# Kernel tuning notes

Measured on AMD Instinct MI355X. Metric: run time of the kernel, lower is better.

Reference implementation:

```python
import jax, jax.numpy as jnp
import numpy as np

H = 16  # num_heads


def setup_inputs() -> dict:
    key = jax.random.key(0)
    ks = jax.random.split(key, 8)
    B, S, d, L = 1, 2048, 1024, 8
    hd = d // H
    s = 0.02
    return {
        "x": jax.random.normal(ks[0], (B, S, d), jnp.float32),
        "past_values": jax.random.normal(ks[1], (L, B, H, S, hd), jnp.float32),
        "Wqkv": jax.random.normal(ks[2], (3 * d, d), jnp.float32) * s,
        "bqkv": jax.random.normal(ks[3], (3 * d,), jnp.float32) * s,
        "Wcol": jax.random.normal(ks[4], (d, d), jnp.float32) * s,
        "bcol": jax.random.normal(ks[5], (d,), jnp.float32) * s,
        "Wout": jax.random.normal(ks[6], (d, d), jnp.float32) * s,
        "bout": jax.random.normal(ks[7], (d,), jnp.float32) * s,
    }


def reference(x, past_values, Wqkv, bqkv, Wcol, bcol, Wout, bout):
    B, S, d = x.shape
    L = past_values.shape[0]
    hd = d // H
    scale = 1.0 / np.sqrt(hd).astype(np.float32)

    qkv = x @ Wqkv.T + bqkv                       # [B,S,3d]
    q, k, v = jnp.split(qkv, 3, axis=-1)

    def heads(t):                                  # [B,S,d] -> [B,H,S,hd]
        return t.reshape(B, S, H, hd).transpose(0, 2, 1, 3)

    q_row, k, v = heads(q), heads(k), heads(v)
    q_col = heads(x @ Wcol.T + bcol)

    # causal token scores [B,H,S,S]
    token_scores = jnp.einsum('bhqd,bhkd->bhqk', q_row, k) * scale
    causal = jnp.triu(jnp.ones((S, S), bool), 1)
    token_scores = jnp.where(causal, -jnp.inf, token_scores)

    # stack past values: torch stack(dim=3) -> [B,H,S,L,hd]; permute -> [B,S,L,H*hd]
    pv = past_values.transpose(1, 3, 0, 2, 4).reshape(B, S, L, d)
    ri = pv.reshape(B, S * L, d)
    mu = ri.mean(-1, keepdims=True)
    var = ri.var(-1, keepdims=True)
    ri = (ri - mu) / jnp.sqrt(var + 1e-5)          # F.layer_norm, no affine

    Wk, bk = Wqkv[d:2 * d], bqkv[d:2 * d]
    Wv, bv = Wqkv[2 * d:], bqkv[2 * d:]
    rk = (ri @ Wk.T + bk).reshape(B, S * L, H, hd).transpose(0, 2, 1, 3).reshape(B, H, S, L, hd)
    rv = (ri @ Wv.T + bv).reshape(B, S * L, H, hd).transpose(0, 2, 1, 3).reshape(B, H, S, L, hd)

    mem_scores = jnp.einsum('bhsd,bhsld->bhsl', q_col, rk) * scale  # [B,H,S,L]

    scores = jnp.concatenate([token_scores, mem_scores], axis=-1)   # [B,H,S,S+L]
    w = jax.nn.softmax(scores, axis=-1)
    tw, mw = w[..., :S], w[..., S:]

    ctx = jnp.einsum('bhqk,bhkd->bhqd', tw, v) + jnp.einsum('bhsl,bhsld->bhsd', mw, rv)
    out = ctx.transpose(0, 2, 1, 3).reshape(B, S, d)
    return out @ Wout.T + bout
```

## Files before the change

### kernel.cpp

```cpp
#include <hip/hip_runtime.h>
#include <math.h>

#define D   1024
#define H   16
#define HD  64
#define SEQ 2048
#define LL  8
#define SCALE 0.125f

typedef __attribute__((ext_vector_type(8))) __bf16 bf16x8;
typedef __attribute__((ext_vector_type(4))) float floatx4;
typedef __attribute__((ext_vector_type(8))) unsigned short ushort8;

__device__ inline unsigned short f32_to_bf16(float f) {
    unsigned int u = __builtin_bit_cast(unsigned int, f);
    u += 0x7FFF + ((u >> 16) & 1);
    return (unsigned short)(u >> 16);
}
__device__ inline float bf2f(unsigned short u) {
    unsigned int x = (unsigned int)u << 16;
    return __builtin_bit_cast(float, x);
}
__device__ inline void load_lds16(const void* g, void* l) {
    __builtin_amdgcn_global_load_lds(
        (__attribute__((address_space(1))) void*)g,
        (__attribute__((address_space(3))) void*)l, 16, 0, 0);
}

__device__ inline void xcd_swizzle(int& bx, int& by) {
    const int gx   = gridDim.x;
    const int lin  = blockIdx.y * gx + blockIdx.x;
    const int nblk = gx * gridDim.y;
    const int virt = (lin & 7) * (nblk >> 3) + (lin >> 3);
    bx = virt % gx;
    by = virt / gx;
}

#define NQ_X    524288
#define NQ_WQKV 786432
#define NQ_WC   262144
#define NQ_WO   262144
#define LN_BLK  16384
#define CVT_BLK 7168
#define PREP_GRID (LN_BLK + CVT_BLK + 4)

__global__ __launch_bounds__(256) void prep_kernel(
    const float* __restrict__ pv, const float* __restrict__ x,
    const float* __restrict__ Wqkv, const float* __restrict__ Wcol,
    const float* __restrict__ Wout, const float* __restrict__ bqkv,
    const float* __restrict__ bcol,
    unsigned short* __restrict__ ri, unsigned short* __restrict__ xb,
    unsigned short* __restrict__ W4b, unsigned short* __restrict__ Woutb,
    float* __restrict__ b4)
{
    const int b = blockIdx.x;
    const int t = threadIdx.x;
    if (b < LN_BLK) {
        const int r = b;
        const int s = r >> 3, l = r & 7;
        const int h = t >> 4, e = (t & 15) * 4;
        const size_t src = (size_t)l * (H * SEQ * HD) + (size_t)h * (SEQ * HD)
                         + (size_t)s * HD + e;
        float4 v = *(const float4*)(pv + src);
        float sum = v.x + v.y + v.z + v.w;
        float sq  = v.x * v.x + v.y * v.y + v.z * v.z + v.w * v.w;
#pragma unroll
        for (int off = 32; off; off >>= 1) {
            sum += __shfl_xor(sum, off);
            sq  += __shfl_xor(sq, off);
        }
        __shared__ float red[8];
        if ((t & 63) == 0) { red[(t >> 6) * 2] = sum; red[(t >> 6) * 2 + 1] = sq; }
        __syncthreads();
        sum = red[0] + red[2] + red[4] + red[6];
        sq  = red[1] + red[3] + red[5] + red[7];
        const float mean = sum * (1.f / 1024.f);
        const float var  = sq * (1.f / 1024.f) - mean * mean;
        const float rstd = rsqrtf(var + 1e-5f);
        ushort4 o;
        o.x = f32_to_bf16((v.x - mean) * rstd);
        o.y = f32_to_bf16((v.y - mean) * rstd);
        o.z = f32_to_bf16((v.z - mean) * rstd);
        o.w = f32_to_bf16((v.w - mean) * rstd);
        *(ushort4*)(ri + (size_t)r * D + t * 4) = o;
    } else if (b < LN_BLK + CVT_BLK) {
        const int i = (b - LN_BLK) * 256 + t;
        const float* src; unsigned short* dst; int off;
        if (i < NQ_X)                        { src = x;    dst = xb;    off = i; }
        else if (i < NQ_X + NQ_WQKV)         { src = Wqkv; dst = W4b;   off = i - NQ_X; }
        else if (i < NQ_X + NQ_WQKV + NQ_WC) {
            float4 v = ((const float4*)Wcol)[i - NQ_X - NQ_WQKV];
            ushort4 o;
            o.x = f32_to_bf16(v.x); o.y = f32_to_bf16(v.y);
            o.z = f32_to_bf16(v.z); o.w = f32_to_bf16(v.w);
            ((ushort4*)(W4b))[NQ_WQKV + (i - NQ_X - NQ_WQKV)] = o;
            return;
        }
        else                                 { src = Wout; dst = Woutb; off = i - NQ_X - NQ_WQKV - NQ_WC; }
        float4 v = ((const float4*)src)[off];
        ushort4 o;
        o.x = f32_to_bf16(v.x); o.y = f32_to_bf16(v.y);
        o.z = f32_to_bf16(v.z); o.w = f32_to_bf16(v.w);
        ((ushort4*)dst)[off] = o;
    } else {
        const int q = (b - LN_BLK - CVT_BLK) * 256 + t;
        float4 v = (q < 768) ? ((const float4*)bqkv)[q] : ((const float4*)bcol)[q - 768];
        ((float4*)b4)[q] = v;
    }
}

__global__ __launch_bounds__(256) void wkt_kernel(
    const float* __restrict__ Wqkv, unsigned short* __restrict__ WkT)
{
    const int h = blockIdx.x >> 4, ct = blockIdx.x & 15;
    const int c0 = ct * 64;
    const int t = threadIdx.x;
    __shared__ float tile[64][68];
    {
        const int e  = t >> 2;
        const int c4 = (t & 3) * 16;
        const float* src = Wqkv + (size_t)(D + h * HD + e) * D + c0 + c4;
#pragma unroll
        for (int j = 0; j < 4; j++) {
            float4 v = ((const float4*)src)[j];
            *(float4*)&tile[e][c4 + j * 4] = v;
        }
    }
    __syncthreads();
    {
        const int c  = t >> 2;
        const int e0 = (t & 3) * 16;
        ushort8 o0, o1;
#pragma unroll
        for (int j = 0; j < 8; j++) o0[j] = f32_to_bf16(tile[e0 + j][c]);
#pragma unroll
        for (int j = 0; j < 8; j++) o1[j] = f32_to_bf16(tile[e0 + 8 + j][c]);
        unsigned short* dst = WkT + (size_t)h * (D * HD) + (size_t)(c0 + c) * HD + e0;
        *(ushort8*)dst       = o0;
        *(ushort8*)(dst + 8) = o1;
    }
}

template <typename CT, bool HAS_BIAS>
__global__ __launch_bounds__(256) void gemm_bf16_kernel(
    const unsigned short* __restrict__ A, const unsigned short* __restrict__ W,
    const float* __restrict__ bias, CT* __restrict__ C,
    int K, int N, int lda, int ldw, int ldc,
    size_t zsA, size_t zsW, size_t zsC)
{
    A += (size_t)blockIdx.z * zsA;
    W += (size_t)blockIdx.z * zsW;
    C += (size_t)blockIdx.z * zsC;

    __shared__ unsigned short As[128 * 32];
    __shared__ unsigned short Ws[128 * 32];
    const int t    = threadIdx.x;
    const int wave = t >> 6, lane = t & 63;
    const int wm   = wave >> 1, wn = wave & 1;
    int bx, by;
    xcd_swizzle(bx, by);
    const int m0 = by * 128, n0 = bx * 128;

    floatx4 acc[4][4];
#pragma unroll
    for (int i = 0; i < 4; i++)
#pragma unroll
        for (int j = 0; j < 4; j++) acc[i][j] = (floatx4)0.f;

    const int lrow = lane >> 2;
    const int lcol = (lane & 3) * 8;
    const unsigned short* Ag = A + (size_t)(m0 + wave * 32 + lrow) * lda + lcol;
    const unsigned short* Wg = W + (size_t)(n0 + wave * 32 + lrow) * ldw + lcol;
    unsigned short* Asw = &As[wave * 32 * 32];
    unsigned short* Wsw = &Ws[wave * 32 * 32];
    const size_t rowskipA = (size_t)16 * lda;
    const size_t rowskipW = (size_t)16 * ldw;

    const int arow  = lane & 15;
    const int aquad = (lane >> 4) * 8;

    for (int k0 = 0; k0 < K; k0 += 32) {
        load_lds16(Ag + k0,             Asw);
        load_lds16(Ag + k0 + rowskipA,  Asw + 16 * 32);
        load_lds16(Wg + k0,             Wsw);
        load_lds16(Wg + k0 + rowskipW,  Wsw + 16 * 32);
        __syncthreads();

        bf16x8 af[4], wf[4];
#pragma unroll
        for (int mi = 0; mi < 4; mi++)
            af[mi] = *(const bf16x8*)&As[(wm * 64 + mi * 16 + arow) * 32 + aquad];
#pragma unroll
        for (int ni = 0; ni < 4; ni++)
            wf[ni] = *(const bf16x8*)&Ws[(wn * 64 + ni * 16 + arow) * 32 + aquad];
#pragma unroll
        for (int mi = 0; mi < 4; mi++)
#pragma unroll
            for (int ni = 0; ni < 4; ni++)
                acc[mi][ni] = __builtin_amdgcn_mfma_f32_16x16x32_bf16(
                    af[mi], wf[ni], acc[mi][ni], 0, 0, 0);
        __syncthreads();
    }

    const int crow = (lane >> 4) * 4, ccol = lane & 15;
#pragma unroll
    for (int mi = 0; mi < 4; mi++) {
#pragma unroll
        for (int ni = 0; ni < 4; ni++) {
            const int gm = m0 + wm * 64 + mi * 16 + crow;
            const int gn = n0 + wn * 64 + ni * 16 + ccol;
            float bb = 0.f;
            if constexpr (HAS_BIAS) bb = bias[gn];
#pragma unroll
            for (int r = 0; r < 4; r++) {
                float v = acc[mi][ni][r] + bb;
                if constexpr (sizeof(CT) == 2)
                    C[(size_t)(gm + r) * ldc + gn] = (CT)f32_to_bf16(v);
                else
                    C[(size_t)(gm + r) * ldc + gn] = v;
            }
        }
    }
}

#define RI_STRIDE 1032

__global__ __launch_bounds__(256) void memsc_kernel(
    const unsigned short* __restrict__ U, const unsigned short* __restrict__ ri,
    const unsigned short* __restrict__ qkv4, const float* __restrict__ bqkv,
    float* __restrict__ scores)
{
    const int s = blockIdx.x;
    const int t = threadIdx.x;
    __shared__ unsigned short riS[LL * RI_STRIDE];
    __shared__ float qbS[H];
    {
        const unsigned short* src = ri + (size_t)s * (LL * D);
#pragma unroll
        for (int j = 0; j < 4; j++) {
            const int off = (j * 256 + t) * 8;
            const int l = off >> 10, c = off & 1023;
            ushort8 v = *(const ushort8*)(src + off);
            *(ushort8*)&riS[l * RI_STRIDE + c] = v;
        }
    }
    {
        const int h = t >> 4, sub = t & 15;
        const unsigned short* qc = qkv4 + (size_t)s * 4096 + 3 * D + h * HD + sub * 4;
        const float* bk = bqkv + D + h * HD + sub * 4;
        float acc = 0.f;
#pragma unroll
        for (int j = 0; j < 4; j++) acc += bf2f(qc[j]) * bk[j];
#pragma unroll
        for (int off = 1; off < 16; off <<= 1) acc += __shfl_xor(acc, off);
        if (sub == 0) qbS[h] = acc;
    }
    __syncthreads();
    const int p = t >> 1, half = t & 1;
    const int h = p >> 3, l = p & 7;
    const unsigned short* Up = U + ((size_t)h * SEQ + s) * D + half * 512;
    const unsigned short* rp = &riS[l * RI_STRIDE + half * 512];
    float acc = 0.f;
#pragma unroll 4
    for (int j = 0; j < 64; j++) {
        ushort8 u = *(const ushort8*)(Up + j * 8);
        ushort8 r = *(const ushort8*)(rp + j * 8);
#pragma unroll
        for (int k = 0; k < 8; k++) acc += bf2f(u[k]) * bf2f(r[k]);
    }
    acc += __shfl_xor(acc, 1);
    if (half == 0)
        scores[((size_t)s * H + h) * LL + l] = (acc + qbS[h]) * SCALE;
}

union AttnShared {
    struct { unsigned short Qs[64 * 72]; unsigned short Ks[64 * 72]; } qk;
    float Osp[64 * 68];
};

__global__ __launch_bounds__(256) void attn_split_kernel(
    const unsigned short* __restrict__ qkv4,
    const float* __restrict__ mem_scores, float* __restrict__ memP,
    float* __restrict__ Opart, float2* __restrict__ mlpart)
{
    const int t    = threadIdx.x;
    const int w    = t >> 6, lane = t & 63;
    const int lrow = lane & 15;
    const int lk   = (lane >> 4) * 8;
    const int rrow = (lane >> 4) * 4;
    const int lin  = blockIdx.x;
    const int hs   = lin & 31, g = lin >> 5;
    const int h    = hs >> 1, s = hs & 1;
    const int a    = g & 7, bq = g >> 3;
    const int qt   = (bq == 0) ? a : (bq == 1) ? 15 - a : (bq == 2) ? 16 + a : 31 - a;
    const int q0   = qt * 64;
    const int n    = qt + 1, nh = (n + 1) >> 1;
    const int lo   = s ? nh : 0, hi = s ? n : nh;
    const int part = (h * 32 + qt) * 2 + s;

    __shared__ AttnShared U;
    __shared__ unsigned short Vt[64 * 72];
    __shared__ unsigned short Pb[64 * 72];
    __shared__ float row_m[64], row_l[64];
    __shared__ float mem_mm[64], mem_alpha[64], mem_suml[64];

#pragma unroll
    for (int p = 0; p < 2; p++) {
        int idx = p * 256 + t;
        int row = idx >> 3, col = (idx & 7) * 8;
        *(bf16x8*)&U.qk.Qs[row * 72 + col] =
            *(const bf16x8*)(qkv4 + (size_t)(q0 + row) * 4096 + h * HD + col);
    }

    float m_i[4], l_i[4];
    floatx4 Oacc[4];
#pragma unroll
    for (int r = 0; r < 4; r++) { m_i[r] = -1e30f; l_i[r] = 0.f; }
#pragma unroll
    for (int et = 0; et < 4; et++) Oacc[et] = (floatx4)0.f;

    for (int jt = lo; jt < hi; jt++) {
        const int j0 = jt * 64;
#pragma unroll
        for (int p = 0; p < 2; p++) {
            int idx = p * 256 + t;
            int row = idx >> 3, col = (idx & 7) * 8;
            *(bf16x8*)&U.qk.Ks[row * 72 + col] =
                *(const bf16x8*)(qkv4 + (size_t)(j0 + row) * 4096 + D + h * HD + col);
        }
        {
            const int pr = t & 31, eg = t >> 5;
            const unsigned short* v0 =
                qkv4 + (size_t)(j0 + 2 * pr) * 4096 + 2 * D + h * HD + eg * 8;
            ushort8 va = *(const ushort8*)v0;
            ushort8 vb = *(const ushort8*)(v0 + 4096);
#pragma unroll
            for (int j = 0; j < 8; j++) {
                unsigned int pk = (unsigned int)va[j] | ((unsigned int)vb[j] << 16);
                *(unsigned int*)&Vt[(eg * 8 + j) * 72 + 2 * pr] = pk;
            }
        }
        __syncthreads();

        floatx4 S[4];
#pragma unroll
        for (int nt = 0; nt < 4; nt++) S[nt] = (floatx4)0.f;
#pragma unroll
        for (int kst = 0; kst < 2; kst++) {
            bf16x8 aq = *(const bf16x8*)&U.qk.Qs[(w * 16 + lrow) * 72 + kst * 32 + lk];
#pragma unroll
            for (int nt = 0; nt < 4; nt++) {
                bf16x8 bk = *(const bf16x8*)&U.qk.Ks[(nt * 16 + lrow) * 72 + kst * 32 + lk];
                S[nt] = __builtin_amdgcn_mfma_f32_16x16x32_bf16(aq, bk, S[nt], 0, 0, 0);
            }
        }

#pragma unroll
        for (int r = 0; r < 4; r++) {
            const int qg = q0 + w * 16 + rrow + r;
            float sc[4];
            float mx = -1e30f;
#pragma unroll
            for (int nt = 0; nt < 4; nt++) {
                sc[nt] = S[nt][r] * SCALE;
                if (j0 + nt * 16 + lrow > qg) sc[nt] = -1e30f;
                mx = fmaxf(mx, sc[nt]);
            }
#pragma unroll
            for (int off = 1; off < 16; off <<= 1)
                mx = fmaxf(mx, __shfl_xor(mx, off));
            if (mx <= -1e29f) {
#pragma unroll
                for (int nt = 0; nt < 4; nt++)
                    Pb[(w * 16 + rrow + r) * 72 + nt * 16 + lrow] = 0;
                continue;
            }
            const float newm  = fmaxf(m_i[r], mx);
            const float alpha = __expf(m_i[r] - newm);
            m_i[r] = newm;
            float ps = 0.f;
#pragma unroll
            for (int nt = 0; nt < 4; nt++) {
                float pe = __expf(sc[nt] - newm);
                ps += pe;
                Pb[(w * 16 + rrow + r) * 72 + nt * 16 + lrow] = f32_to_bf16(pe);
            }
#pragma unroll
            for (int off = 1; off < 16; off <<= 1)
                ps += __shfl_xor(ps, off);
            l_i[r] = l_i[r] * alpha + ps;
#pragma unroll
            for (int et = 0; et < 4; et++) Oacc[et][r] *= alpha;
        }
        __syncthreads();

#pragma unroll
        for (int kst = 0; kst < 2; kst++) {
            bf16x8 ap = *(const bf16x8*)&Pb[(w * 16 + lrow) * 72 + kst * 32 + lk];
#pragma unroll
            for (int et = 0; et < 4; et++) {
                bf16x8 bv = *(const bf16x8*)&Vt[(et * 16 + lrow) * 72 + kst * 32 + lk];
                Oacc[et] = __builtin_amdgcn_mfma_f32_16x16x32_bf16(ap, bv, Oacc[et], 0, 0, 0);
            }
        }
        __syncthreads();
    }

    if (s == 1) {
#pragma unroll
        for (int r = 0; r < 4; r++) {
            const int ql = w * 16 + rrow + r;
            if (lrow == 0) mlpart[(size_t)part * 64 + ql] = make_float2(m_i[r], l_i[r]);
#pragma unroll
            for (int et = 0; et < 4; et++)
                Opart[((size_t)part * 64 + ql) * 64 + et * 16 + lrow] = Oacc[et][r];
        }
        return;
    }

#pragma unroll
    for (int r = 0; r < 4; r++) {
        const int ql = w * 16 + rrow + r;
        if (lrow == 0) { row_m[ql] = m_i[r]; row_l[ql] = l_i[r]; }
#pragma unroll
        for (int et = 0; et < 4; et++)
            U.Osp[ql * 68 + et * 16 + lrow] = Oacc[et][r];
    }
    __syncthreads();

    if (t < 64) {
        const int qi = t, qg = q0 + qi;
        const float* msp = mem_scores + ((size_t)qg * H + h) * LL;
        float ms[LL];
#pragma unroll
        for (int l = 0; l < LL; l++) ms[l] = msp[l];
        const float mo = row_m[qi];
        float mm = mo;
#pragma unroll
        for (int l = 0; l < LL; l++) mm = fmaxf(mm, ms[l]);
        const float alpha = __expf(mo - mm);
        float suml = 0.f;
        float* mp = memP + ((size_t)qg * H + h) * LL;
#pragma unroll
        for (int l = 0; l < LL; l++) {
            float pe = __expf(ms[l] - mm);
            suml += pe;
            mp[l] = pe;
        }
        mem_mm[qi] = mm; mem_alpha[qi] = alpha; mem_suml[qi] = suml;
    }
    __syncthreads();

    {
        const int tx = t & 15, ty = t >> 4;
#pragma unroll
        for (int i = 0; i < 4; i++) {
            const int qi = ty * 4 + i;
            const float alpha = mem_alpha[qi];
            const float lf = row_l[qi] * alpha + mem_suml[qi];
            float4 o = *(const float4*)&U.Osp[qi * 68 + tx * 4];
            o.x *= alpha; o.y *= alpha; o.z *= alpha; o.w *= alpha;
            *(float4*)&Opart[((size_t)part * 64 + qi) * 64 + tx * 4] = o;
            if (tx == 0) mlpart[(size_t)part * 64 + qi] = make_float2(mem_mm[qi], lf);
        }
    }
}

__global__ __launch_bounds__(256) void attn_merge_kernel(
    const float* __restrict__ Opart, const float2* __restrict__ mlpart,
    const float* __restrict__ memP,
    float* __restrict__ tok, float* __restrict__ mwf, float* __restrict__ Pmem)
{
    const int blk = blockIdx.x;
    const int h = blk >> 5, qt = blk & 31;
    const int q0 = qt * 64;
    const int t = threadIdx.x, tx = t & 15, ty = t >> 4;
    const size_t p0 = (size_t)blk * 2, p1 = p0 + 1;
#pragma unroll
    for (int i = 0; i < 4; i++) {
        const int qi = ty * 4 + i, qg = q0 + qi;
        float2 ml0 = mlpart[p0 * 64 + qi];
        float2 ml1 = mlpart[p1 * 64 + qi];
        const float M  = fmaxf(ml0.x, ml1.x);
        const float f0 = __expf(ml0.x - M), f1 = __expf(ml1.x - M);
        const float rl = 1.f / (ml0.y * f0 + ml1.y * f1);
        float4 o0 = *(const float4*)&Opart[(p0 * 64 + qi) * 64 + tx * 4];
        float4 o1 = *(const float4*)&Opart[(p1 * 64 + qi) * 64 + tx * 4];
        float4 o;
        o.x = (o0.x * f0 + o1.x * f1) * rl;
        o.y = (o0.y * f0 + o1.y * f1) * rl;
        o.z = (o0.z * f0 + o1.z * f1) * rl;
        o.w = (o0.w * f0 + o1.w * f1) * rl;
        *(float4*)&tok[(size_t)qg * D + h * HD + tx * 4] = o;
        if (tx == 0) {
            const float w0 = f0 * rl;
            const float* mp = memP + ((size_t)qg * H + h) * LL;
            float* mw = mwf + ((size_t)qg * H + h) * LL;
            float psum = 0.f;
#pragma unroll
            for (int l = 0; l < LL; l++) { float v = mp[l] * w0; mw[l] = v; psum += v; }
            Pmem[(size_t)qg * H + h] = psum;
        }
    }
}

__global__ __launch_bounds__(256) void rbar_kernel(
    const float* __restrict__ mwf, const unsigned short* __restrict__ ri,
    unsigned short* __restrict__ rbar)
{
    const int s = blockIdx.x, t = threadIdx.x;
    __shared__ unsigned short riS[LL * D];
    __shared__ float wS[H * LL];
    {
        const unsigned short* src = ri + (size_t)s * (LL * D);
#pragma unroll
        for (int j = 0; j < 4; j++) {
            const int off = (j * 256 + t) * 8;
            *(ushort8*)&riS[off] = *(const ushort8*)(src + off);
        }
    }
    if (t < H * LL) wS[t] = mwf[(size_t)s * (H * LL) + t];
    __syncthreads();
    const int c4 = t * 4;
#pragma unroll
    for (int hh = 0; hh < H; hh++) {
        float v0 = 0.f, v1 = 0.f, v2 = 0.f, v3 = 0.f;
#pragma unroll
        for (int l = 0; l < LL; l++) {
            const float wv = wS[hh * LL + l];
            ushort4 rr = *(const ushort4*)&riS[l * D + c4];
            v0 += wv * bf2f(rr.x); v1 += wv * bf2f(rr.y);
            v2 += wv * bf2f(rr.z); v3 += wv * bf2f(rr.w);
        }
        ushort4 o;
        o.x = f32_to_bf16(v0); o.y = f32_to_bf16(v1);
        o.z = f32_to_bf16(v2); o.w = f32_to_bf16(v3);
        *(ushort4*)(rbar + ((size_t)hh * SEQ + s) * D + c4) = o;
    }
}

__global__ __launch_bounds__(256) void gemm_ctx_kernel(
    const unsigned short* __restrict__ rbar, const unsigned short* __restrict__ W4,
    const float* __restrict__ bqkv, const float* __restrict__ Pmem,
    const float* __restrict__ tok, unsigned short* __restrict__ ctx)
{
    const int mt = blockIdx.x;
    const int h  = blockIdx.y;
    const unsigned short* A  = rbar + (size_t)h * SEQ * D + (size_t)mt * 128 * D;
    const unsigned short* Wv = W4 + (size_t)(2 * D + h * HD) * D;
    const float* bv = bqkv + 2 * D + h * HD;

    __shared__ unsigned short As[128 * 32];
    __shared__ unsigned short Ws[64 * 32];
    const int t    = threadIdx.x;
    const int wave = t >> 6, lane = t & 63;

    floatx4 acc[2][4];
#pragma unroll
    for (int i = 0; i < 2; i++)
#pragma unroll
        for (int j = 0; j < 4; j++) acc[i][j] = (floatx4)0.f;

    const int lrow = lane >> 2;
    const int lcol = (lane & 3) * 8;
    const unsigned short* Ag = A  + (size_t)(wave * 32 + lrow) * D + lcol;
    const unsigned short* Wg = Wv + (size_t)(wave * 32 + lrow) * D + lcol;
    unsigned short* Asw = &As[wave * 32 * 32];
    unsigned short* Wsw = &Ws[wave * 32 * 32];
    const size_t rowskip = (size_t)16 * D;

    const int arow  = lane & 15;
    const int aquad = (lane >> 4) * 8;

    for (int k0 = 0; k0 < D; k0 += 32) {
        load_lds16(Ag + k0,           Asw);
        load_lds16(Ag + k0 + rowskip, Asw + 16 * 32);
        if (wave < 2) {
            load_lds16(Wg + k0,           Wsw);
            load_lds16(Wg + k0 + rowskip, Wsw + 16 * 32);
        }
        __syncthreads();

        bf16x8 af[2], wf[4];
#pragma unroll
        for (int mi = 0; mi < 2; mi++)
            af[mi] = *(const bf16x8*)&As[(wave * 32 + mi * 16 + arow) * 32 + aquad];
#pragma unroll
        for (int ni = 0; ni < 4; ni++)
            wf[ni] = *(const bf16x8*)&Ws[(ni * 16 + arow) * 32 + aquad];
#pragma unroll
        for (int mi = 0; mi < 2; mi++)
#pragma unroll
            for (int ni = 0; ni < 4; ni++)
                acc[mi][ni] = __builtin_amdgcn_mfma_f32_16x16x32_bf16(
                    af[mi], wf[ni], acc[mi][ni], 0, 0, 0);
        __syncthreads();
    }

    const int crow = (lane >> 4) * 4, ccol = lane & 15;
#pragma unroll
    for (int mi = 0; mi < 2; mi++) {
#pragma unroll
        for (int ni = 0; ni < 4; ni++) {
            const int e  = ni * 16 + ccol;
            const float bb = bv[e];
#pragma unroll
            for (int r = 0; r < 4; r++) {
                const int grow = mt * 128 + wave * 32 + mi * 16 + crow + r;
                float v = acc[mi][ni][r] + bb * Pmem[(size_t)grow * H + h]
                          + tok[(size_t)grow * D + h * HD + e];
                ctx[(size_t)grow * D + h * HD + e] = f32_to_bf16(v);
            }
        }
    }
}

extern "C" void kernel_launch(void* const* d_in, const int* in_sizes, int n_in,
                              void* d_out, int out_size, void* d_ws, size_t ws_size,
                              hipStream_t stream)
{
    const float* x    = (const float*)d_in[0];
    const float* pv   = (const float*)d_in[1];
    const float* Wqkv = (const float*)d_in[2];
    const float* bqkv = (const float*)d_in[3];
    const float* Wcol = (const float*)d_in[4];
    const float* bcol = (const float*)d_in[5];
    const float* Wout = (const float*)d_in[6];
    const float* bout = (const float*)d_in[7];
    float* out = (float*)d_out;

    char* p = (char*)d_ws;
    unsigned short* x_bf    = (unsigned short*)p; p += (size_t)2048 * 1024 * 2;
    unsigned short* W4_bf   = (unsigned short*)p; p += (size_t)4096 * 1024 * 2;
    unsigned short* Wout_bf = (unsigned short*)p; p += (size_t)1024 * 1024 * 2;
    float*          b4      = (float*)p;          p += (size_t)4096 * 4;
    unsigned short* ri_bf   = (unsigned short*)p; p += (size_t)16384 * 1024 * 2;
    unsigned short* qkv4_bf = (unsigned short*)p; p += (size_t)2048 * 4096 * 2;
    unsigned short* WkT_bf  = (unsigned short*)p; p += (size_t)16 * 1024 * 64 * 2;
    float*          scores  = (float*)p;          p += (size_t)2048 * 16 * 8 * 4;
    float*          memP    = (float*)p;          p += (size_t)2048 * 16 * 8 * 4;
    float*          mwf     = (float*)p;          p += (size_t)2048 * 16 * 8 * 4;
    float*          Pmem    = (float*)p;          p += (size_t)2048 * 16 * 4;
    float*          tok     = (float*)p;          p += (size_t)2048 * 1024 * 4;
    unsigned short* ctx_bf  = (unsigned short*)p; p += (size_t)2048 * 1024 * 2;
    float*          Opart   = (float*)p;          p += (size_t)1024 * 64 * 64 * 4;
    float2*         mlpart  = (float2*)p;         p += (size_t)1024 * 64 * 8;
    unsigned short* Urb     = (unsigned short*)p; p += (size_t)16 * 2048 * 1024 * 2;

    prep_kernel<<<PREP_GRID, 256, 0, stream>>>(pv, x, Wqkv, Wcol, Wout, bqkv, bcol,
                                               ri_bf, x_bf, W4_bf, Wout_bf, b4);
    wkt_kernel<<<256, 256, 0, stream>>>(Wqkv, WkT_bf);
    gemm_bf16_kernel<unsigned short, true><<<dim3(32, 16, 1), 256, 0, stream>>>(
        x_bf, W4_bf, b4, qkv4_bf, 1024, 4096, 1024, 1024, 4096, 0, 0, 0);
    gemm_bf16_kernel<unsigned short, false><<<dim3(8, 16, 16), 256, 0, stream>>>(
        qkv4_bf + 3 * D, WkT_bf, nullptr, Urb, 64, 1024, 4096, 64, 1024,
        (size_t)HD, (size_t)D * HD, (size_t)SEQ * D);
    memsc_kernel<<<2048, 256, 0, stream>>>(Urb, ri_bf, qkv4_bf, bqkv, scores);
    attn_split_kernel<<<1024, 256, 0, stream>>>(qkv4_bf, scores, memP, Opart, mlpart);
    attn_merge_kernel<<<512, 256, 0, stream>>>(Opart, mlpart, memP, tok, mwf, Pmem);
    rbar_kernel<<<2048, 256, 0, stream>>>(mwf, ri_bf, Urb);
    gemm_ctx_kernel<<<dim3(16, 16), 256, 0, stream>>>(Urb, W4_bf, bqkv, Pmem, tok, ctx_bf);
    gemm_bf16_kernel<float, true><<<dim3(8, 16, 1), 256, 0, stream>>>(
        ctx_bf, Wout_bf, bout, out, 1024, 1024, 1024, 1024, 1024, 0, 0, 0);
}
```

Before: 365.5 us.

## Split attention KV range four ways with register-prefetched K/V and Q in registers

The causal attention kernel now splits each (head, query-tile) KV range into four parts instead of two, doubling the grid to 2048 blocks, and the merge kernel combines four partials. Q fragments are held in registers rather than LDS. The next K/V tile is prefetched into registers while the current tile is computed. MFMA sections are wrapped in s_setprio, and the final partial output is written straight from registers instead of staged through shared memory. The aim is better load balance and latency hiding in the attention stage, at the cost of more partial-result traffic, more register pressure, and a heavier merge.

Measured after the change: 343.7 us. -5.9%, faster.

```diff
diff --git a/kernel.cpp b/kernel.cpp
--- a/kernel.cpp
+++ b/kernel.cpp
@@ -273,11 +273,6 @@
         scores[((size_t)s * H + h) * LL + l] = (acc + qbS[h]) * SCALE;
 }
 
-union AttnShared {
-    struct { unsigned short Qs[64 * 72]; unsigned short Ks[64 * 72]; } qk;
-    float Osp[64 * 68];
-};
-
 __global__ __launch_bounds__(256) void attn_split_kernel(
     const unsigned short* __restrict__ qkv4,
     const float* __restrict__ mem_scores, float* __restrict__ memP,
@@ -289,28 +284,30 @@
     const int lk   = (lane >> 4) * 8;
     const int rrow = (lane >> 4) * 4;
     const int lin  = blockIdx.x;
-    const int hs   = lin & 31, g = lin >> 5;
-    const int h    = hs >> 1, s = hs & 1;
+    const int hsp  = lin & 63, g = lin >> 6;
+    const int h    = hsp >> 2, s = hsp & 3;
     const int a    = g & 7, bq = g >> 3;
     const int qt   = (bq == 0) ? a : (bq == 1) ? 15 - a : (bq == 2) ? 16 + a : 31 - a;
     const int q0   = qt * 64;
-    const int n    = qt + 1, nh = (n + 1) >> 1;
-    const int lo   = s ? nh : 0, hi = s ? n : nh;
-    const int part = (h * 32 + qt) * 2 + s;
-
-    __shared__ AttnShared U;
+    const int n    = qt + 1;
+    const int lo   = (s * n) >> 2, hi = ((s + 1) * n) >> 2;
+    const int part = (h * 32 + qt) * 4 + s;
+
+    __shared__ unsigned short Ks[64 * 72];
     __shared__ unsigned short Vt[64 * 72];
     __shared__ unsigned short Pb[64 * 72];
     __shared__ float row_m[64], row_l[64];
     __shared__ float mem_mm[64], mem_alpha[64], mem_suml[64];
 
-#pragma unroll
-    for (int p = 0; p < 2; p++) {
-        int idx = p * 256 + t;
-        int row = idx >> 3, col = (idx & 7) * 8;
-        *(bf16x8*)&U.qk.Qs[row * 72 + col] =
-            *(const bf16x8*)(qkv4 + (size_t)(q0 + row) * 4096 + h * HD + col);
-    }
+    bf16x8 qreg[2];
+#pragma unroll
+    for (int kst = 0; kst < 2; kst++)
+        qreg[kst] = *(const bf16x8*)(qkv4 + (size_t)(q0 + w * 16 + lrow) * 4096
+                                     + h * HD + kst * 32 + lk);
+
+    bf16x8 kr[2];
+    ushort8 va, vb;
+    const int vpr = t & 31, veg = t >> 5;
 
     float m_i[4], l_i[4];
     floatx4 Oacc[4];
@@ -319,41 +316,58 @@
 #pragma unroll
     for (int et = 0; et < 4; et++) Oacc[et] = (floatx4)0.f;
 
+    const int krow = (t >> 3);
+    const int kcol = (t & 7) * 8;
+
+    if (lo < hi) {
+        const int j0 = lo * 64;
+#pragma unroll
+        for (int p = 0; p < 2; p++)
+            kr[p] = *(const bf16x8*)(qkv4 + (size_t)(j0 + p * 32 + krow) * 4096
+                                     + D + h * HD + kcol);
+        const unsigned short* v0 =
+            qkv4 + (size_t)(j0 + 2 * vpr) * 4096 + 2 * D + h * HD + veg * 8;
+        va = *(const ushort8*)v0;
+        vb = *(const ushort8*)(v0 + 4096);
+#pragma unroll
+        for (int p = 0; p < 2; p++)
+            *(bf16x8*)&Ks[(p * 32 + krow) * 72 + kcol] = kr[p];
+#pragma unroll
+        for (int j = 0; j < 8; j++) {
+            unsigned int pk = (unsigned int)va[j] | ((unsigned int)vb[j] << 16);
+            *(unsigned int*)&Vt[(veg * 8 + j) * 72 + 2 * vpr] = pk;
+        }
+        __syncthreads();
+    }
+
     for (int jt = lo; jt < hi; jt++) {
         const int j0 = jt * 64;
-#pragma unroll
-        for (int p = 0; p < 2; p++) {
-            int idx = p * 256 + t;
-            int row = idx >> 3, col = (idx & 7) * 8;
-            *(bf16x8*)&U.qk.Ks[row * 72 + col] =
-                *(const bf16x8*)(qkv4 + (size_t)(j0 + row) * 4096 + D + h * HD + col);
-        }
-        {
-            const int pr = t & 31, eg = t >> 5;
+        const bool pf = (jt + 1 < hi);
+        if (pf) {
+            const int j0n = (jt + 1) * 64;
+#pragma unroll
+            for (int p = 0; p < 2; p++)
+                kr[p] = *(const bf16x8*)(qkv4 + (size_t)(j0n + p * 32 + krow) * 4096
+                                         + D + h * HD + kcol);
             const unsigned short* v0 =
-                qkv4 + (size_t)(j0 + 2 * pr) * 4096 + 2 * D + h * HD + eg * 8;
-            ushort8 va = *(const ushort8*)v0;
-            ushort8 vb = *(const ushort8*)(v0 + 4096);
-#pragma unroll
-            for (int j = 0; j < 8; j++) {
-                unsigned int pk = (unsigned int)va[j] | ((unsigned int)vb[j] << 16);
-                *(unsigned int*)&Vt[(eg * 8 + j) * 72 + 2 * pr] = pk;
-            }
-        }
-        __syncthreads();
+                qkv4 + (size_t)(j0n + 2 * vpr) * 4096 + 2 * D + h * HD + veg * 8;
+            va = *(const ushort8*)v0;
+            vb = *(const ushort8*)(v0 + 4096);
+        }
 
         floatx4 S[4];
 #pragma unroll
         for (int nt = 0; nt < 4; nt++) S[nt] = (floatx4)0.f;
+        __builtin_amdgcn_s_setprio(1);
 #pragma unroll
         for (int kst = 0; kst < 2; kst++) {
-            bf16x8 aq = *(const bf16x8*)&U.qk.Qs[(w * 16 + lrow) * 72 + kst * 32 + lk];
 #pragma unroll
             for (int nt = 0; nt < 4; nt++) {
-                bf16x8 bk = *(const bf16x8*)&U.qk.Ks[(nt * 16 + lrow) * 72 + kst * 32 + lk];
-                S[nt] = __builtin_amdgcn_mfma_f32_16x16x32_bf16(aq, bk, S[nt], 0, 0, 0);
-            }
-        }
+                bf16x8 bk = *(const bf16x8*)&Ks[(nt * 16 + lrow) * 72 + kst * 32 + lk];
+                S[nt] = __builtin_amdgcn_mfma_f32_16x16x32_bf16(qreg[kst], bk, S[nt], 0, 0, 0);
+            }
+        }
+        __builtin_amdgcn_s_setprio(0);
 
 #pragma unroll
         for (int r = 0; r < 4; r++) {
@@ -392,8 +406,8 @@
 #pragma unroll
             for (int et = 0; et < 4; et++) Oacc[et][r] *= alpha;
         }
-        __syncthreads();
-
+
+        __builtin_amdgcn_s_setprio(1);
 #pragma unroll
         for (int kst = 0; kst < 2; kst++) {
             bf16x8 ap = *(const bf16x8*)&Pb[(w * 16 + lrow) * 72 + kst * 32 + lk];
@@ -403,10 +417,23 @@
                 Oacc[et] = __builtin_amdgcn_mfma_f32_16x16x32_bf16(ap, bv, Oacc[et], 0, 0, 0);
             }
         }
-        __syncthreads();
-    }
-
-    if (s == 1) {
+        __builtin_amdgcn_s_setprio(0);
+
+        if (pf) {
+            __syncthreads();
+#pragma unroll
+            for (int p = 0; p < 2; p++)
+                *(bf16x8*)&Ks[(p * 32 + krow) * 72 + kcol] = kr[p];
+#pragma unroll
+            for (int j = 0; j < 8; j++) {
+                unsigned int pk = (unsigned int)va[j] | ((unsigned int)vb[j] << 16);
+                *(unsigned int*)&Vt[(veg * 8 + j) * 72 + 2 * vpr] = pk;
+            }
+            __syncthreads();
+        }
+    }
+
+    if (s != 0) {
 #pragma unroll
         for (int r = 0; r < 4; r++) {
             const int ql = w * 16 + rrow + r;
@@ -422,9 +449,6 @@
     for (int r = 0; r < 4; r++) {
         const int ql = w * 16 + rrow + r;
         if (lrow == 0) { row_m[ql] = m_i[r]; row_l[ql] = l_i[r]; }
-#pragma unroll
-        for (int et = 0; et < 4; et++)
-            U.Osp[ql * 68 + et * 16 + lrow] = Oacc[et][r];
     }
     __syncthreads();
 
@@ -451,18 +475,16 @@
     }
     __syncthreads();
 
-    {
-        const int tx = t & 15, ty = t >> 4;
-#pragma unroll
-        for (int i = 0; i < 4; i++) {
-            const int qi = ty * 4 + i;
-            const float alpha = mem_alpha[qi];
-            const float lf = row_l[qi] * alpha + mem_suml[qi];
-            float4 o = *(const float4*)&U.Osp[qi * 68 + tx * 4];
-            o.x *= alpha; o.y *= alpha; o.z *= alpha; o.w *= alpha;
-            *(float4*)&Opart[((size_t)part * 64 + qi) * 64 + tx * 4] = o;
-            if (tx == 0) mlpart[(size_t)part * 64 + qi] = make_float2(mem_mm[qi], lf);
-        }
+#pragma unroll
+    for (int r = 0; r < 4; r++) {
+        const int ql = w * 16 + rrow + r;
+        const float alpha = mem_alpha[ql];
+        if (lrow == 0)
+            mlpart[(size_t)part * 64 + ql] =
+                make_float2(mem_mm[ql], l_i[r] * alpha + mem_suml[ql]);
+#pragma unroll
+        for (int et = 0; et < 4; et++)
+            Opart[((size_t)part * 64 + ql) * 64 + et * 16 + lrow] = Oacc[et][r] * alpha;
     }
 }
 
@@ -475,25 +497,30 @@
     const int h = blk >> 5, qt = blk & 31;
     const int q0 = qt * 64;
     const int t = threadIdx.x, tx = t & 15, ty = t >> 4;
-    const size_t p0 = (size_t)blk * 2, p1 = p0 + 1;
+    const size_t pb = (size_t)blk * 4;
 #pragma unroll
     for (int i = 0; i < 4; i++) {
         const int qi = ty * 4 + i, qg = q0 + qi;
-        float2 ml0 = mlpart[p0 * 64 + qi];
-        float2 ml1 = mlpart[p1 * 64 + qi];
-        const float M  = fmaxf(ml0.x, ml1.x);
-        const float f0 = __expf(ml0.x - M), f1 = __expf(ml1.x - M);
-        const float rl = 1.f / (ml0.y * f0 + ml1.y * f1);
-        float4 o0 = *(const float4*)&Opart[(p0 * 64 + qi) * 64 + tx * 4];
-        float4 o1 = *(const float4*)&Opart[(p1 * 64 + qi) * 64 + tx * 4];
-        float4 o;
-        o.x = (o0.x * f0 + o1.x * f1) * rl;
-        o.y = (o0.y * f0 + o1.y * f1) * rl;
-        o.z = (o0.z * f0 + o1.z * f1) * rl;
-        o.w = (o0.w * f0 + o1.w * f1) * rl;
+        float2 ml[4];
+#pragma unroll
+        for (int ps = 0; ps < 4; ps++) ml[ps] = mlpart[(pb + ps) * 64 + qi];
+        float M = ml[0].x;
+#pragma unroll
+        for (int ps = 1; ps < 4; ps++) M = fmaxf(M, ml[ps].x);
+        float f[4], L = 0.f;
+#pragma unroll
+        for (int ps = 0; ps < 4; ps++) { f[ps] = __expf(ml[ps].x - M); L += ml[ps].y * f[ps]; }
+        const float rl = 1.f / L;
+        float4 o = make_float4(0.f, 0.f, 0.f, 0.f);
+#pragma unroll
+        for (int ps = 0; ps < 4; ps++) {
+            const float fs = f[ps] * rl;
+            float4 op = *(const float4*)&Opart[((pb + ps) * 64 + qi) * 64 + tx * 4];
+            o.x += op.x * fs; o.y += op.y * fs; o.z += op.z * fs; o.w += op.w * fs;
+        }
         *(float4*)&tok[(size_t)qg * D + h * HD + tx * 4] = o;
         if (tx == 0) {
-            const float w0 = f0 * rl;
+            const float w0 = f[0] * rl;
             const float* mp = memP + ((size_t)qg * H + h) * LL;
             float* mw = mwf + ((size_t)qg * H + h) * LL;
             float psum = 0.f;
@@ -643,8 +670,8 @@
     float*          Pmem    = (float*)p;          p += (size_t)2048 * 16 * 4;
     float*          tok     = (float*)p;          p += (size_t)2048 * 1024 * 4;
     unsigned short* ctx_bf  = (unsigned short*)p; p += (size_t)2048 * 1024 * 2;
-    float*          Opart   = (float*)p;          p += (size_t)1024 * 64 * 64 * 4;
-    float2*         mlpart  = (float2*)p;         p += (size_t)1024 * 64 * 8;
+    float*          Opart   = (float*)p;          p += (size_t)2048 * 64 * 64 * 4;
+    float2*         mlpart  = (float2*)p;         p += (size_t)2048 * 64 * 8;
     unsigned short* Urb     = (unsigned short*)p; p += (size_t)16 * 2048 * 1024 * 2;
 
     prep_kernel<<<PREP_GRID, 256, 0, stream>>>(pv, x, Wqkv, Wcol, Wout, bqkv, bcol,
@@ -656,7 +683,7 @@
         qkv4_bf + 3 * D, WkT_bf, nullptr, Urb, 64, 1024, 4096, 64, 1024,
         (size_t)HD, (size_t)D * HD, (size_t)SEQ * D);
     memsc_kernel<<<2048, 256, 0, stream>>>(Urb, ri_bf, qkv4_bf, bqkv, scores);
-    attn_split_kernel<<<1024, 256, 0, stream>>>(qkv4_bf, scores, memP, Opart, mlpart);
+    attn_split_kernel<<<2048, 256, 0, stream>>>(qkv4_bf, scores, memP, Opart, mlpart);
     attn_merge_kernel<<<512, 256, 0, stream>>>(Opart, mlpart, memP, tok, mwf, Pmem);
     rbar_kernel<<<2048, 256, 0, stream>>>(mwf, ri_bf, Urb);
     gemm_ctx_kernel<<<dim3(16, 16), 256, 0, stream>>>(Urb, W4_bf, bqkv, Pmem, tok, ctx_bf);
```
